# Optimization experiments

Hardware: AMD Instinct MI355X
Metric: run time of the kernel (lower is better)

Reference implementation:

```python
import jax, jax.numpy as jnp
import numpy as np

N_NODES = 50000
N_EDGES = 1_600_000
D_IN, D_HID, D_OUT = 512, 256, 64


def setup_inputs() -> dict:
    key = jax.random.key(0)
    ks = jax.random.split(key, 8)
    x = jax.random.normal(ks[0], (N_NODES, D_IN), dtype=jnp.float32)
    edge_rows = jax.random.randint(ks[1], (N_EDGES,), 0, N_NODES, dtype=jnp.int32)
    edge_cols = jax.random.randint(ks[2], (N_EDGES,), 0, N_NODES, dtype=jnp.int32)
    # normalized adjacency values (e.g. D^-1/2 A D^-1/2 entries)
    edge_vals = jax.random.uniform(ks[3], (N_EDGES,), dtype=jnp.float32)
    W1 = jax.random.normal(ks[4], (D_IN, D_HID), dtype=jnp.float32) * (1.0 / np.sqrt(D_IN))
    b1 = jnp.zeros((D_HID,), dtype=jnp.float32)
    W2 = jax.random.normal(ks[5], (D_HID, D_OUT), dtype=jnp.float32) * (1.0 / np.sqrt(D_HID))
    b2 = jnp.zeros((D_OUT,), dtype=jnp.float32)
    return {"x": x, "edge_rows": edge_rows, "edge_cols": edge_cols,
            "edge_vals": edge_vals, "W1": W1, "b1": b1, "W2": W2, "b2": b2}


def _spmm(rows, cols, vals, h):
    # out[r] = sum_{e: rows[e]==r} vals[e] * h[cols[e]]
    msgs = vals[:, None] * h[cols]          # [E, d] gather
    return jax.ops.segment_sum(msgs, rows, num_segments=N_NODES)


def reference(x, edge_rows, edge_cols, edge_vals, W1, b1, W2, b2):
    h = x @ W1 + b1                          # W1(x)
    h = _spmm(edge_rows, edge_cols, edge_vals, h)  # sparse.mm(A_hat, h)
    h = jax.nn.relu(h)                       # relu; dropout is identity in eval
    h = h @ W2 + b2                           # W2(h)
    out = _spmm(edge_rows, edge_cols, edge_vals, h)
    return out
```

## Files before the change

### kernel.cpp

```cpp
#include <hip/hip_runtime.h>
#include <hip/hip_bf16.h>

constexpr int NN = 50000;
constexpr int NE = 1600000;
constexpr int DI = 512;
constexpr int DH = 256;
constexpr int DO = 64;

constexpr int NC = NN * 16;
constexpr int G1_BLOCKS = ((NN + 127) / 128) * (DH / 128);
constexpr int SC_BLOCKS = 2048;
constexpr int SCAN_BLOCKS = (NN + 1023) / 1024;
constexpr int E4_CAP = NE + NN * 16 + 64;

typedef __attribute__((ext_vector_type(8))) short short8;
typedef __attribute__((ext_vector_type(4))) float f32x4;

__device__ inline ushort f2b(float f) {
    uint u = __float_as_uint(f);
    u += 0x7fffu + ((u >> 16) & 1u);
    return (ushort)(u >> 16);
}
__device__ inline float b2f(ushort u) {
    return __uint_as_float((uint)u << 16);
}
__device__ inline void gload16(const void* g, void* l) {
    __builtin_amdgcn_global_load_lds(
        (const __attribute__((address_space(1))) unsigned int*)g,
        (__attribute__((address_space(3))) unsigned int*)l, 16, 0, 0);
}


__global__ void k_prep(const float* __restrict__ X, ushort* __restrict__ Xb,
                       const float* __restrict__ W1, ushort* __restrict__ w1bT,
                       const float* __restrict__ W2, ushort* __restrict__ w2bT,
                       const int* __restrict__ er, const int* __restrict__ ec,
                       const float* __restrict__ ev,
                       int* __restrict__ counts2, uint* __restrict__ rc32,
                       ushort* __restrict__ evb) {
    const int bid = blockIdx.x;
    const int tid = threadIdx.x;
    if (bid < 1024) {
        const float4* x4 = (const float4*)X;
        ushort4* o4 = (ushort4*)Xb;
        const int stride = 1024 * 256;
        for (int i = bid * 256 + tid; i < NN * DI / 4; i += stride) {
            float4 v = x4[i];
            o4[i] = make_ushort4(f2b(v.x), f2b(v.y), f2b(v.z), f2b(v.w));
        }
    } else {
        const int b = bid - 1024;
        const int stride = 1024 * 256;
        const int4* r4 = (const int4*)er;
        const int4* c4 = (const int4*)ec;
        const float4* v4 = (const float4*)ev;
        for (int i = b * 256 + tid; i < NE / 4; i += stride) {
            int4 r = r4[i];
            int4 c = c4[i];
            float4 v = v4[i];
            *(uint4*)&rc32[i * 4] = make_uint4(
                ((uint)r.x << 16) | (uint)c.x, ((uint)r.y << 16) | (uint)c.y,
                ((uint)r.z << 16) | (uint)c.z, ((uint)r.w << 16) | (uint)c.w);
            *(ushort4*)&evb[i * 4] =
                make_ushort4(f2b(v.x), f2b(v.y), f2b(v.z), f2b(v.w));
            atomicAdd(&counts2[(r.x << 4) | (c.x >> 12)], 1);
            atomicAdd(&counts2[(r.y << 4) | (c.y >> 12)], 1);
            atomicAdd(&counts2[(r.z << 4) | (c.z >> 12)], 1);
            atomicAdd(&counts2[(r.w << 4) | (c.w >> 12)], 1);
        }
        for (int i = b * 256 + tid; i < DI * DH; i += stride) {
            int n = i >> 9, k = i & 511;
            w1bT[i] = f2b(W1[(size_t)k * DH + n]);
        }
        for (int i = b * 256 + tid; i < DH * DO; i += stride) {
            int n = i >> 8, k = i & 255;
            w2bT[i] = f2b(W2[(size_t)k * DO + n]);
        }
    }
}


__global__ __launch_bounds__(1024) void k_scanA(const int* __restrict__ counts2,
                                                int* __restrict__ rp,
                                                int* __restrict__ partials) {
    const int t = threadIdx.x;
    const int r = blockIdx.x * 1024 + t;
    int s = 0;
    if (r < NN) {
        const int4* c4 = (const int4*)(counts2 + (size_t)r * 16);
        int4 a = c4[0], b = c4[1], c = c4[2], d = c4[3];
        s = a.x + a.y + a.z + a.w + b.x + b.y + b.z + b.w
          + c.x + c.y + c.z + c.w + d.x + d.y + d.z + d.w;
        s = (s + 15) & ~15;
    }
    __shared__ int buf[1024];
    buf[t] = s;
    __syncthreads();
    for (int off = 1; off < 1024; off <<= 1) {
        int v = (t >= off) ? buf[t - off] : 0;
        __syncthreads();
        buf[t] += v;
        __syncthreads();
    }
    if (r < NN) rp[r] = buf[t] - s;
    if (t == 1023) partials[blockIdx.x] = buf[1023];
}

__global__ __launch_bounds__(64) void k_scanB(int* __restrict__ partials,
                                              int* __restrict__ rp) {
    __shared__ int buf[64];
    int t = threadIdx.x;
    int v = (t < SCAN_BLOCKS) ? partials[t] : 0;
    buf[t] = v;
    __syncthreads();
    for (int off = 1; off < 64; off <<= 1) {
        int x = (t >= off) ? buf[t - off] : 0;
        __syncthreads();
        buf[t] += x;
        __syncthreads();
    }
    if (t < SCAN_BLOCKS) partials[t] = buf[t] - v;
    if (t == 63) rp[NN] = buf[63];
}

__global__ __launch_bounds__(1024) void k_scanC(const int* __restrict__ counts2,
                                                int* __restrict__ rp,
                                                int* __restrict__ cur2,
                                                const int* __restrict__ partials) {
    const int t = threadIdx.x;
    const int r = blockIdx.x * 1024 + t;
    if (r < NN) {
        const int off = partials[blockIdx.x];
        const int base = rp[r] + off;
        rp[r] = base;
        const int4* c4 = (const int4*)(counts2 + (size_t)r * 16);
        int4 ca = c4[0], cb = c4[1], cc = c4[2], cd = c4[3];
        int cnt[16] = {ca.x, ca.y, ca.z, ca.w, cb.x, cb.y, cb.z, cb.w,
                       cc.x, cc.y, cc.z, cc.w, cd.x, cd.y, cd.z, cd.w};
        int out[16];
        int rs = 0;
        #pragma unroll
        for (int b = 0; b < 16; ++b) { out[b] = base + rs; rs += cnt[b]; }
        int4* o4 = (int4*)(cur2 + (size_t)r * 16);
        o4[0] = make_int4(out[0],  out[1],  out[2],  out[3]);
        o4[1] = make_int4(out[4],  out[5],  out[6],  out[7]);
        o4[2] = make_int4(out[8],  out[9],  out[10], out[11]);
        o4[3] = make_int4(out[12], out[13], out[14], out[15]);
    }
}


__global__ __launch_bounds__(256, 4) void k_gemm1(const ushort* __restrict__ Xb,
                                                  const ushort* __restrict__ w1bT,
                                                  const float* __restrict__ B,
                                                  ushort* __restrict__ H) {
    __shared__ ushort As[128 * 32];
    __shared__ ushort Bs[128 * 32];
    const int bid = blockIdx.x;
    const int bm = (bid >> 1) * 128;
    const int bn = (bid & 1) * 128;
    const int tid = threadIdx.x;
    const int wid = tid >> 6, lane = tid & 63;
    const int wm = wid >> 1, wn = wid & 1;
    const int lr = lane & 15, lg = lane >> 4;
    const int swz = (lg ^ (lr & 3)) * 8;

    f32x4 acc[4][4];
    #pragma unroll
    for (int i = 0; i < 4; ++i)
        #pragma unroll
        for (int j = 0; j < 4; ++j)
            acc[i][j] = (f32x4){0.f, 0.f, 0.f, 0.f};

    for (int kt = 0; kt < DI; kt += 32) {
        #pragma unroll
        for (int c = 0; c < 2; ++c) {
            int i = c * 256 + tid;
            int row = i >> 2, slot = i & 3;
            int ss = slot ^ (row & 3);
            const ushort* g = Xb + (size_t)(bm + row) * DI + kt + ss * 8;
            gload16(g, As + (size_t)(c * 256 + wid * 64) * 8);
        }
        #pragma unroll
        for (int c = 0; c < 2; ++c) {
            int i = c * 256 + tid;
            int row = i >> 2, slot = i & 3;
            int ss = slot ^ (row & 3);
            const ushort* g = w1bT + (size_t)(bn + row) * DI + kt + ss * 8;
            gload16(g, Bs + (size_t)(c * 256 + wid * 64) * 8);
        }
        __syncthreads();

        short8 a[4], b[4];
        #pragma unroll
        for (int f = 0; f < 4; ++f) {
            a[f] = *(short8*)&As[(wm * 64 + f * 16 + lr) * 32 + swz];
            b[f] = *(short8*)&Bs[(wn * 64 + f * 16 + lr) * 32 + swz];
        }
        #pragma unroll
        for (int i = 0; i < 4; ++i)
            #pragma unroll
            for (int j = 0; j < 4; ++j)
                acc[i][j] = __builtin_amdgcn_mfma_f32_16x16x32_bf16(a[i], b[j], acc[i][j], 0, 0, 0);
        __syncthreads();
    }

    #pragma unroll
    for (int i = 0; i < 4; ++i) {
        int r0 = bm + wm * 64 + i * 16 + lg * 4;
        #pragma unroll
        for (int j = 0; j < 4; ++j) {
            int col = bn + wn * 64 + j * 16 + lr;
            float bias = B[col];
            #pragma unroll
            for (int e = 0; e < 4; ++e) {
                int r = r0 + e;
                if (r < NN) H[(size_t)r * DH + col] = f2b(acc[i][j][e] + bias);
            }
        }
    }
}


__global__ __launch_bounds__(256) void k_scatter(const uint* __restrict__ rc32,
                                                 const ushort* __restrict__ evb,
                                                 int* __restrict__ cur2,
                                                 uint* __restrict__ e4) {
    const int g = blockIdx.x & 7;
    const uint lo = g * (NN / 8), hi = lo + (NN / 8);
    const uint4* rc4 = (const uint4*)rc32;
    for (int q = (blockIdx.x >> 3) * 256 + (int)threadIdx.x; q < NE / 4;
         q += (SC_BLOCKS / 8) * 256) {
        uint4 t = rc4[q];
        #pragma unroll
        for (int e = 0; e < 4; ++e) {
            uint rc = (e == 0) ? t.x : (e == 1) ? t.y : (e == 2) ? t.z : t.w;
            uint rr = rc >> 16;
            if (rr >= lo && rr < hi) {
                uint c = rc & 0xffffu;
                uint vb = evb[q * 4 + e];
                int p = atomicAdd(&cur2[(rr << 4) | (c >> 12)], 1);
                e4[p] = c | (vb << 16);
            }
        }
    }
}


__global__ __launch_bounds__(256) void k_srg(const int* __restrict__ rp,
                                             const uint* __restrict__ e4,
                                             const ushort* __restrict__ H,
                                             const ushort* __restrict__ w2bT,
                                             const float* __restrict__ B2,
                                             ushort* __restrict__ H2) {
    __shared__ ushort hs[16][264];
    const int tid = threadIdx.x;
    const int w = tid >> 6, lane = tid & 63;
    const int half = lane >> 5;
    const int dl = lane & 31;
    const ushort* gbase = H + dl * 8;
    const uint4* eq = (const uint4*)e4;

    #pragma unroll
    for (int q = 0; q < 4; ++q) {
        const int r = blockIdx.x * 16 + w * 4 + q;
        const int s = rp[r], e = rp[r + 1];
        float a[8] = {0.f, 0.f, 0.f, 0.f, 0.f, 0.f, 0.f, 0.f};

        int qi = s >> 2;
        uint4 q0 = eq[qi], q1 = eq[qi + 1], q2 = eq[qi + 2], q3 = eq[qi + 3];
        for (int i = s; i < e; i += 16) {
            uint u[8];
            u[0] = half ? q0.y : q0.x;  u[1] = half ? q0.w : q0.z;
            u[2] = half ? q1.y : q1.x;  u[3] = half ? q1.w : q1.z;
            u[4] = half ? q2.y : q2.x;  u[5] = half ? q2.w : q2.z;
            u[6] = half ? q3.y : q3.x;  u[7] = half ? q3.w : q3.z;
            uint4 hw[8];
            #pragma unroll
            for (int k = 0; k < 8; ++k)
                hw[k] = *(const uint4*)(gbase + (size_t)(u[k] & 0xffffu) * DH);
            qi += 4;
            q0 = eq[qi]; q1 = eq[qi + 1]; q2 = eq[qi + 2]; q3 = eq[qi + 3];
            #pragma unroll
            for (int k = 0; k < 8; ++k) {
                float v = __uint_as_float(u[k] & 0xffff0000u);
                uint w0 = hw[k].x, w1 = hw[k].y, w2 = hw[k].z, w3 = hw[k].w;
                a[0] += v * __uint_as_float(w0 << 16);
                a[1] += v * __uint_as_float(w0 & 0xffff0000u);
                a[2] += v * __uint_as_float(w1 << 16);
                a[3] += v * __uint_as_float(w1 & 0xffff0000u);
                a[4] += v * __uint_as_float(w2 << 16);
                a[5] += v * __uint_as_float(w2 & 0xffff0000u);
                a[6] += v * __uint_as_float(w3 << 16);
                a[7] += v * __uint_as_float(w3 & 0xffff0000u);
            }
        }
        #pragma unroll
        for (int d = 0; d < 8; ++d) a[d] += __shfl_xor(a[d], 32);
        if (half == 0) {
            short8 o;
            #pragma unroll
            for (int d = 0; d < 8; ++d) o[d] = (short)f2b(fmaxf(a[d], 0.f));
            *(short8*)&hs[w * 4 + q][dl * 8] = o;
        }
    }
    __syncthreads();

    const int lr = lane & 15, lg = lane >> 4;
    f32x4 acc = (f32x4){0.f, 0.f, 0.f, 0.f};
    #pragma unroll
    for (int kt = 0; kt < DH; kt += 32) {
        short8 af = *(short8*)&hs[lr][kt + lg * 8];
        short8 bf = *(const short8*)(w2bT + (size_t)(w * 16 + lr) * DH + kt + lg * 8);
        acc = __builtin_amdgcn_mfma_f32_16x16x32_bf16(af, bf, acc, 0, 0, 0);
    }
    const int col = w * 16 + lr;
    const float bias = B2[col];
    #pragma unroll
    for (int e = 0; e < 4; ++e) {
        int row = blockIdx.x * 16 + lg * 4 + e;
        H2[(size_t)row * DO + col] = f2b(acc[e] + bias);
    }
}


__global__ __launch_bounds__(256) void k_spmm_out(const int* __restrict__ rp,
                                                  const uint* __restrict__ e4,
                                                  const ushort* __restrict__ H2,
                                                  float* __restrict__ OUT) {
    const int r = blockIdx.x * 4 + (threadIdx.x >> 6);
    const int lane = threadIdx.x & 63;
    const int slot = lane >> 3;
    const int dq = lane & 7;
    const int s = rp[r], e = rp[r + 1];
    const ushort* base = H2 + dq * 8;
    float a[8] = {0.f, 0.f, 0.f, 0.f, 0.f, 0.f, 0.f, 0.f};

    for (int i = s; i < e; i += 16) {
        uint2 u = *(const uint2*)(e4 + i + 2 * slot);
        short8 h0 = *(const short8*)(base + (size_t)(u.x & 0xffffu) * DO);
        short8 h1 = *(const short8*)(base + (size_t)(u.y & 0xffffu) * DO);
        float v0 = __uint_as_float(u.x & 0xffff0000u);
        float v1 = __uint_as_float(u.y & 0xffff0000u);
        #pragma unroll
        for (int d = 0; d < 8; ++d)
            a[d] += v0 * b2f((ushort)h0[d]) + v1 * b2f((ushort)h1[d]);
    }
    #pragma unroll
    for (int d = 0; d < 8; ++d) {
        a[d] += __shfl_xor(a[d], 8);
        a[d] += __shfl_xor(a[d], 16);
        a[d] += __shfl_xor(a[d], 32);
    }
    if (slot == 0) {
        float* o = OUT + (size_t)r * DO + dq * 8;
        *(float4*)o       = make_float4(a[0], a[1], a[2], a[3]);
        *(float4*)(o + 4) = make_float4(a[4], a[5], a[6], a[7]);
    }
}


extern "C" void kernel_launch(void* const* d_in, const int* in_sizes, int n_in,
                              void* d_out, int out_size, void* d_ws, size_t ws_size,
                              hipStream_t stream) {
    const float* x  = (const float*)d_in[0];
    const int*   er = (const int*)d_in[1];
    const int*   ec = (const int*)d_in[2];
    const float* ev = (const float*)d_in[3];
    const float* W1 = (const float*)d_in[4];
    const float* b1 = (const float*)d_in[5];
    const float* W2 = (const float*)d_in[6];
    const float* b2 = (const float*)d_in[7];
    float* out = (float*)d_out;

    char* ws = (char*)d_ws;
    ushort* Xb  = (ushort*)ws;
    uint*   e4  = (uint*)ws;
    ws += (size_t)NN * DI * 2;
    ushort* h1  = (ushort*)ws; ws += (size_t)NN * DH * 2;
    ushort* h2  = (ushort*)ws;
    uint*   rc32 = (uint*)ws;  ws += (size_t)NN * DO * 2;
    int* counts2 = (int*)ws;   ws += ((size_t)NC * 4 + 255) & ~(size_t)255;
    int* rp     = (int*)ws;    ws += ((size_t)(NN + 1) * 4 + 255) & ~(size_t)255;
    int* cur2   = (int*)ws;    ws += ((size_t)NC * 4 + 255) & ~(size_t)255;
    int* partials = (int*)ws;  ws += 256;
    ushort* w1bT = (ushort*)ws; ws += ((size_t)DI * DH * 2 + 255) & ~(size_t)255;
    ushort* w2bT = (ushort*)ws; ws += ((size_t)DH * DO * 2 + 255) & ~(size_t)255;
    ushort* evb  = (ushort*)ws; ws += ((size_t)NE * 2 + 255) & ~(size_t)255;

    hipMemsetAsync(counts2, 0, (size_t)NC * 4, stream);
    k_prep<<<2048, 256, 0, stream>>>(x, Xb, W1, w1bT, W2, w2bT,
                                     er, ec, ev, counts2, rc32, evb);
    k_scanA<<<SCAN_BLOCKS, 1024, 0, stream>>>(counts2, rp, partials);
    k_scanB<<<1, 64, 0, stream>>>(partials, rp);
    k_scanC<<<SCAN_BLOCKS, 1024, 0, stream>>>(counts2, rp, cur2, partials);
    k_gemm1<<<G1_BLOCKS, 256, 0, stream>>>(Xb, w1bT, b1, h1);
    hipMemsetAsync(e4, 0, (size_t)E4_CAP * 4, stream);
    k_scatter<<<SC_BLOCKS, 256, 0, stream>>>(rc32, evb, cur2, e4);
    k_srg<<<NN / 16, 256, 0, stream>>>(rp, e4, h1, w2bT, b2, h2);
    k_spmm_out<<<NN / 4, 256, 0, stream>>>(rp, e4, h2, out);
}
```

Baseline: 322.7 us.

## Split fused SpMM+GEMM2 into feature-segmented SpMM and separate MFMA GEMM

Replaces the fused first-layer aggregation plus W2 projection kernel with two kernels. The new SpMM assigns each of 8 blocks in a group one 32-column slice of the hidden features, so concurrently running blocks share a narrower gather footprint that may stay cache-resident, and it prefetches edge entries with nontemporal loads. A standalone 128-row-tile MFMA GEMM then applies W2 and the bias. This adds a round trip of the intermediate hidden matrix through global memory and re-reads the edge list eight times.

```diff
diff --git a/kernel.cpp b/kernel.cpp
--- a/kernel.cpp
+++ b/kernel.cpp
@@ -13,8 +13,13 @@
 constexpr int SCAN_BLOCKS = (NN + 1023) / 1024;
 constexpr int E4_CAP = NE + NN * 16 + 64;
 
+constexpr int SP1_BLOCKS = 2048;
+constexpr int SP1_GROUPS = SP1_BLOCKS / 8;
+constexpr int SP1_RPG = (NN + SP1_GROUPS - 1) / SP1_GROUPS;
+
 typedef __attribute__((ext_vector_type(8))) short short8;
 typedef __attribute__((ext_vector_type(4))) float f32x4;
+typedef __attribute__((ext_vector_type(2))) uint uint2v;
 
 __device__ inline ushort f2b(float f) {
     uint u = __float_as_uint(f);
@@ -247,79 +252,95 @@
 }
 
 
-__global__ __launch_bounds__(256) void k_srg(const int* __restrict__ rp,
-                                             const uint* __restrict__ e4,
-                                             const ushort* __restrict__ H,
-                                             const ushort* __restrict__ w2bT,
-                                             const float* __restrict__ B2,
-                                             ushort* __restrict__ H2) {
-    __shared__ ushort hs[16][264];
+__global__ __launch_bounds__(256, 8) void k_spmm1s(const int* __restrict__ rp,
+                                                   const uint* __restrict__ e4,
+                                                   const ushort* __restrict__ H,
+                                                   ushort* __restrict__ O) {
+    const int seg = blockIdx.x & 7;
+    const int grp = blockIdx.x >> 3;
+    const int w = threadIdx.x >> 6, lane = threadIdx.x & 63;
+    const int slot = lane >> 3;
+    const int dq = lane & 7;
+    const ushort* gbase = H + seg * 32 + dq * 4;
+    const int r1 = min(grp * SP1_RPG + SP1_RPG, NN);
+
+    for (int r = grp * SP1_RPG + w; r < r1; r += 4) {
+        const int s = rp[r], e = rp[r + 1];
+        float a0 = 0.f, a1 = 0.f, a2 = 0.f, a3 = 0.f;
+        uint2v u = __builtin_nontemporal_load((const uint2v*)(e4 + s + 2 * slot));
+        for (int i = s; i < e; i += 16) {
+            uint2v uc = u;
+            if (i + 16 < e)
+                u = __builtin_nontemporal_load((const uint2v*)(e4 + i + 16 + 2 * slot));
+            ushort4 h0 = *(const ushort4*)(gbase + (size_t)(uc.x & 0xffffu) * DH);
+            ushort4 h1 = *(const ushort4*)(gbase + (size_t)(uc.y & 0xffffu) * DH);
+            float v0 = __uint_as_float(uc.x & 0xffff0000u);
+            float v1 = __uint_as_float(uc.y & 0xffff0000u);
+            a0 += v0 * b2f(h0.x) + v1 * b2f(h1.x);
+            a1 += v0 * b2f(h0.y) + v1 * b2f(h1.y);
+            a2 += v0 * b2f(h0.z) + v1 * b2f(h1.z);
+            a3 += v0 * b2f(h0.w) + v1 * b2f(h1.w);
+        }
+        #pragma unroll
+        for (int m = 8; m < 64; m <<= 1) {
+            a0 += __shfl_xor(a0, m); a1 += __shfl_xor(a1, m);
+            a2 += __shfl_xor(a2, m); a3 += __shfl_xor(a3, m);
+        }
+        if (slot == 0) {
+            ushort4 o = make_ushort4(f2b(fmaxf(a0, 0.f)), f2b(fmaxf(a1, 0.f)),
+                                     f2b(fmaxf(a2, 0.f)), f2b(fmaxf(a3, 0.f)));
+            *(ushort4*)(O + (size_t)r * DH + seg * 32 + dq * 4) = o;
+        }
+    }
+}
+
+
+__global__ __launch_bounds__(256) void k_gemm2(const ushort* __restrict__ HB,
+                                               const ushort* __restrict__ w2bT,
+                                               const float* __restrict__ B2,
+                                               ushort* __restrict__ H2) {
     const int tid = threadIdx.x;
-    const int w = tid >> 6, lane = tid & 63;
-    const int half = lane >> 5;
-    const int dl = lane & 31;
-    const ushort* gbase = H + dl * 8;
-    const uint4* eq = (const uint4*)e4;
-
+    const int wid = tid >> 6, lane = tid & 63;
+    const int lr = lane & 15, lg = lane >> 4;
+    const int r0 = blockIdx.x * 128 + wid * 32;
+
+    f32x4 acc[2][4];
     #pragma unroll
-    for (int q = 0; q < 4; ++q) {
-        const int r = blockIdx.x * 16 + w * 4 + q;
-        const int s = rp[r], e = rp[r + 1];
-        float a[8] = {0.f, 0.f, 0.f, 0.f, 0.f, 0.f, 0.f, 0.f};
-
-        int qi = s >> 2;
-        uint4 q0 = eq[qi], q1 = eq[qi + 1], q2 = eq[qi + 2], q3 = eq[qi + 3];
-        for (int i = s; i < e; i += 16) {
-            uint u[8];
-            u[0] = half ? q0.y : q0.x;  u[1] = half ? q0.w : q0.z;
-            u[2] = half ? q1.y : q1.x;  u[3] = half ? q1.w : q1.z;
-            u[4] = half ? q2.y : q2.x;  u[5] = half ? q2.w : q2.z;
-            u[6] = half ? q3.y : q3.x;  u[7] = half ? q3.w : q3.z;
-            uint4 hw[8];
+    for (int i = 0; i < 2; ++i)
+        #pragma unroll
+        for (int j = 0; j < 4; ++j)
+            acc[i][j] = (f32x4){0.f, 0.f, 0.f, 0.f};
+
+    for (int kt = 0; kt < DH; kt += 32) {
+        short8 a[2], b[4];
+        #pragma unroll
+        for (int f = 0; f < 2; ++f) {
+            int row = r0 + f * 16 + lr;
+            a[f] = (row < NN) ? *(const short8*)(HB + (size_t)row * DH + kt + lg * 8)
+                              : (short8){0,0,0,0,0,0,0,0};
+        }
+        #pragma unroll
+        for (int j = 0; j < 4; ++j)
+            b[j] = *(const short8*)(w2bT + (size_t)(j * 16 + lr) * DH + kt + lg * 8);
+        #pragma unroll
+        for (int i = 0; i < 2; ++i)
             #pragma unroll
-            for (int k = 0; k < 8; ++k)
-                hw[k] = *(const uint4*)(gbase + (size_t)(u[k] & 0xffffu) * DH);
-            qi += 4;
-            q0 = eq[qi]; q1 = eq[qi + 1]; q2 = eq[qi + 2]; q3 = eq[qi + 3];
+            for (int j = 0; j < 4; ++j)
+                acc[i][j] = __builtin_amdgcn_mfma_f32_16x16x32_bf16(a[i], b[j], acc[i][j], 0, 0, 0);
+    }
+
+    #pragma unroll
+    for (int i = 0; i < 2; ++i) {
+        #pragma unroll
+        for (int j = 0; j < 4; ++j) {
+            int col = j * 16 + lr;
+            float bias = B2[col];
             #pragma unroll
-            for (int k = 0; k < 8; ++k) {
-                float v = __uint_as_float(u[k] & 0xffff0000u);
-                uint w0 = hw[k].x, w1 = hw[k].y, w2 = hw[k].z, w3 = hw[k].w;
-                a[0] += v * __uint_as_float(w0 << 16);
-                a[1] += v * __uint_as_float(w0 & 0xffff0000u);
-                a[2] += v * __uint_as_float(w1 << 16);
-                a[3] += v * __uint_as_float(w1 & 0xffff0000u);
-                a[4] += v * __uint_as_float(w2 << 16);
-                a[5] += v * __uint_as_float(w2 & 0xffff0000u);
-                a[6] += v * __uint_as_float(w3 << 16);
-                a[7] += v * __uint_as_float(w3 & 0xffff0000u);
+            for (int e = 0; e < 4; ++e) {
+                int row = r0 + i * 16 + lg * 4 + e;
+                if (row < NN) H2[(size_t)row * DO + col] = f2b(acc[i][j][e] + bias);
             }
         }
-        #pragma unroll
-        for (int d = 0; d < 8; ++d) a[d] += __shfl_xor(a[d], 32);
-        if (half == 0) {
-            short8 o;
-            #pragma unroll
-            for (int d = 0; d < 8; ++d) o[d] = (short)f2b(fmaxf(a[d], 0.f));
-            *(short8*)&hs[w * 4 + q][dl * 8] = o;
-        }
-    }
-    __syncthreads();
-
-    const int lr = lane & 15, lg = lane >> 4;
-    f32x4 acc = (f32x4){0.f, 0.f, 0.f, 0.f};
-    #pragma unroll
-    for (int kt = 0; kt < DH; kt += 32) {
-        short8 af = *(short8*)&hs[lr][kt + lg * 8];
-        short8 bf = *(const short8*)(w2bT + (size_t)(w * 16 + lr) * DH + kt + lg * 8);
-        acc = __builtin_amdgcn_mfma_f32_16x16x32_bf16(af, bf, acc, 0, 0, 0);
-    }
-    const int col = w * 16 + lr;
-    const float bias = B2[col];
-    #pragma unroll
-    for (int e = 0; e < 4; ++e) {
-        int row = blockIdx.x * 16 + lg * 4 + e;
-        H2[(size_t)row * DO + col] = f2b(acc[e] + bias);
     }
 }
 
@@ -376,6 +397,7 @@
     char* ws = (char*)d_ws;
     ushort* Xb  = (ushort*)ws;
     uint*   e4  = (uint*)ws;
+    ushort* h1b = (ushort*)(ws + (size_t)12 * 1024 * 1024);
     ws += (size_t)NN * DI * 2;
     ushort* h1  = (ushort*)ws; ws += (size_t)NN * DH * 2;
     ushort* h2  = (ushort*)ws;
@@ -397,6 +419,7 @@
     k_gemm1<<<G1_BLOCKS, 256, 0, stream>>>(Xb, w1bT, b1, h1);
     hipMemsetAsync(e4, 0, (size_t)E4_CAP * 4, stream);
     k_scatter<<<SC_BLOCKS, 256, 0, stream>>>(rc32, evb, cur2, e4);
-    k_srg<<<NN / 16, 256, 0, stream>>>(rp, e4, h1, w2bT, b2, h2);
+    k_spmm1s<<<SP1_BLOCKS, 256, 0, stream>>>(rp, e4, h1, h1b);
+    k_gemm2<<<(NN + 127) / 128, 256, 0, stream>>>(h1b, w2bT, b2, h2);
     k_spmm_out<<<NN / 4, 256, 0, stream>>>(rp, e4, h2, out);
 }
```

After: 410.0 us. 1.27x slower.
